# Kernel optimization log

Measured on AMD Instinct MI355X. Metric: run time of the kernel, lower is better.

The kernel has to match this reference:

```python
import jax, jax.numpy as jnp
import numpy as np

D, L, W_DIM, K = 16, 16, 16, 6
N = D * L * W_DIM
STD_POSITION = 1.0
STD_INTENSITY = 3.0


def _dist_weight():
    # pairwise Gaussian of squared Euclidean distance between voxel coords
    gx, gy, gz = jnp.meshgrid(jnp.arange(D, dtype=jnp.float32),
                              jnp.arange(L, dtype=jnp.float32),
                              jnp.arange(W_DIM, dtype=jnp.float32),
                              indexing='ij')
    sq = jnp.zeros((N, N), dtype=jnp.float32)
    for g in (gx, gy, gz):  # fixed 3-axis loop, accumulate per-axis [N,N] diffs
        v = g.reshape(-1)
        sq = sq + jnp.square(v[:, None] - v[None, :])
    return jnp.exp(-sq / (STD_POSITION ** 2))


def setup_inputs() -> dict:
    key = jax.random.key(0)
    k1, k2 = jax.random.split(key)
    patch = jax.random.uniform(k1, (D, L, W_DIM), dtype=jnp.float32)
    prob = jax.random.uniform(k2, (D, L, W_DIM, K), dtype=jnp.float32)
    return {"patch": patch, "prob": prob, "dist_weight": _dist_weight(), "k": K}


def reference(patch, prob, dist_weight, k):
    f = patch.reshape(-1)  # [N]
    # intensity affinity: exp(-((fi - fj)/std_intensity)^2), detached in original
    intensity = jnp.exp(-jnp.square((f[:, None] - f[None, :]) / STD_INTENSITY))
    weights = jax.lax.stop_gradient(intensity) * dist_weight  # [N, N]
    P = prob.reshape(-1, k)  # [N, K], matches prob[:,:,:,t].reshape(-1)
    WP = weights @ P                       # [N, K]
    num = jnp.sum(P * WP, axis=0)          # sum_ij w_ij p_i p_j per class
    den = P.T @ jnp.sum(weights, axis=1)   # sum_ij w_ij p_i per class
    loss = jnp.float32(k) - jnp.sum(num / den)
    return loss.astype(jnp.float32)
```

## Files before the change

kernel.cpp:

```cpp
#include <hip/hip_runtime.h>

#define KK 6
#define RAD 3
#define NOFF 7
#define NGRP 49
#define NBLK (16 * NGRP)
#define C_INT (-0.16029944898766259f)
#define C_POS (-1.4426950408889634f)

__global__ void __launch_bounds__(256) sncut_main(
    const float* __restrict__ patch,
    const float* __restrict__ prob,
    float* __restrict__ bpart)
{
    const int slice = blockIdx.x / NGRP;
    const int og    = blockIdx.x % NGRP;
    const int dx    = og / NOFF - RAD;
    const int dy    = og % NOFF - RAD;

    const int t = threadIdx.x;
    const int i = (slice << 8) + t;
    const int y = t >> 4, z = t & 15;

    const int xj = slice + dx;
    const int yj = y + dy;
    const bool vxy = ((unsigned)xj < 16u) & ((unsigned)yj < 16u);
    const int jbase = (xj << 8) + (yj << 4);

    const float fi = patch[i];
    const float2* __restrict__ P2 = reinterpret_cast<const float2*>(prob);
    const float2 pi0 = P2[i * 3], pi1 = P2[i * 3 + 1], pi2 = P2[i * 3 + 2];

    const float sqxy = C_POS * (float)(dx * dx + dy * dy);

    float s0 = 0.f, s1 = 0.f, s2 = 0.f, s3 = 0.f, s4 = 0.f, s5 = 0.f, r = 0.f;

    #pragma unroll
    for (int dz = -RAD; dz <= RAD; ++dz) {
        const int zj = z + dz;
        const bool valid = vxy & ((unsigned)zj < 16u);
        const int jj = valid ? (jbase + zj) : i;
        const float fj = patch[jj];
        const float2 q0 = P2[jj * 3], q1 = P2[jj * 3 + 1], q2 = P2[jj * 3 + 2];
        const float df = fi - fj;
        const float sqc = sqxy + (float)(dz * dz) * C_POS;
        float w = exp2f(fmaf(df * df, C_INT, sqc));
        w = valid ? w : 0.f;
        r += w;
        s0 = fmaf(w, q0.x, s0); s1 = fmaf(w, q0.y, s1);
        s2 = fmaf(w, q1.x, s2); s3 = fmaf(w, q1.y, s3);
        s4 = fmaf(w, q2.x, s4); s5 = fmaf(w, q2.y, s5);
    }

    float v[12];
    v[0] = s0 * pi0.x; v[1] = s1 * pi0.y; v[2] = s2 * pi1.x;
    v[3] = s3 * pi1.y; v[4] = s4 * pi2.x; v[5] = s5 * pi2.y;
    v[6] = r * pi0.x;  v[7] = r * pi0.y;  v[8] = r * pi1.x;
    v[9] = r * pi1.y;  v[10] = r * pi2.x; v[11] = r * pi2.y;

    #pragma unroll
    for (int m = 32; m >= 1; m >>= 1) {
        #pragma unroll
        for (int c = 0; c < 12; ++c) v[c] += __shfl_xor(v[c], m);
    }

    __shared__ float ls[4][12];
    const int wave = t >> 6, lane = t & 63;
    if (lane == 0) {
        #pragma unroll
        for (int c = 0; c < 12; ++c) ls[wave][c] = v[c];
    }
    __syncthreads();
    if (t < 12) {
        bpart[blockIdx.x * 12 + t] = ls[0][t] + ls[1][t] + ls[2][t] + ls[3][t];
    }
}

__global__ void __launch_bounds__(256) sncut_final(
    const float* __restrict__ bpart, float* __restrict__ out)
{
    const int t = threadIdx.x;
    float a[12];
    #pragma unroll
    for (int c = 0; c < 12; ++c) a[c] = 0.f;

    for (int row = t; row < NBLK; row += 256) {
        const float4* rp = reinterpret_cast<const float4*>(bpart + row * 12);
        const float4 b0 = rp[0], b1 = rp[1], b2 = rp[2];
        a[0] += b0.x; a[1] += b0.y; a[2]  += b0.z; a[3]  += b0.w;
        a[4] += b1.x; a[5] += b1.y; a[6]  += b1.z; a[7]  += b1.w;
        a[8] += b2.x; a[9] += b2.y; a[10] += b2.z; a[11] += b2.w;
    }

    #pragma unroll
    for (int m = 32; m >= 1; m >>= 1) {
        #pragma unroll
        for (int c = 0; c < 12; ++c) a[c] += __shfl_xor(a[c], m);
    }

    __shared__ float ls[4][12];
    const int wave = t >> 6, lane = t & 63;
    if (lane == 0) {
        #pragma unroll
        for (int c = 0; c < 12; ++c) ls[wave][c] = a[c];
    }
    __syncthreads();
    if (t == 0) {
        float loss = (float)KK;
        #pragma unroll
        for (int c = 0; c < KK; ++c) {
            const float num = ls[0][c]     + ls[1][c]     + ls[2][c]     + ls[3][c];
            const float den = ls[0][c + 6] + ls[1][c + 6] + ls[2][c + 6] + ls[3][c + 6];
            loss -= num / den;
        }
        out[0] = loss;
    }
}

extern "C" void kernel_launch(void* const* d_in, const int* in_sizes, int n_in,
                              void* d_out, int out_size, void* d_ws, size_t ws_size,
                              hipStream_t stream) {
    const float* patch = (const float*)d_in[0];
    const float* prob  = (const float*)d_in[1];
    float* out = (float*)d_out;
    float* bpart = (float*)d_ws;

    sncut_main<<<NBLK, 256, 0, stream>>>(patch, prob, bpart);
    sncut_final<<<1, 256, 0, stream>>>(bpart, out);
}
```

Baseline: 15.54 us.

## Fuse final reduction into main kernel via last-block atomic counter

```diff
diff --git a/kernel.cpp b/kernel.cpp
--- a/kernel.cpp
+++ b/kernel.cpp
@@ -8,9 +8,11 @@
 #define C_INT (-0.16029944898766259f)
 #define C_POS (-1.4426950408889634f)
 
-__global__ void __launch_bounds__(256) sncut_main(
+__global__ void __launch_bounds__(256) sncut_fused(
     const float* __restrict__ patch,
     const float* __restrict__ prob,
+    float* __restrict__ out,
+    unsigned* __restrict__ counter,
     float* __restrict__ bpart)
 {
     const int slice = blockIdx.x / NGRP;
@@ -65,6 +67,7 @@
     }
 
     __shared__ float ls[4][12];
+    __shared__ int lastflag;
     const int wave = t >> 6, lane = t & 63;
     if (lane == 0) {
         #pragma unroll
@@ -72,24 +75,28 @@
     }
     __syncthreads();
     if (t < 12) {
-        bpart[blockIdx.x * 12 + t] = ls[0][t] + ls[1][t] + ls[2][t] + ls[3][t];
+        const float p = ls[0][t] + ls[1][t] + ls[2][t] + ls[3][t];
+        __hip_atomic_store(&bpart[blockIdx.x * 12 + t], p,
+                           __ATOMIC_RELAXED, __HIP_MEMORY_SCOPE_AGENT);
     }
-}
+    __syncthreads();
+    if (t == 0) {
+        const unsigned old = __hip_atomic_fetch_add(
+            counter, 1u, __ATOMIC_ACQ_REL, __HIP_MEMORY_SCOPE_AGENT);
+        lastflag = (old == NBLK - 1) ? 1 : 0;
+    }
+    __syncthreads();
+    if (!lastflag) return;
 
-__global__ void __launch_bounds__(256) sncut_final(
-    const float* __restrict__ bpart, float* __restrict__ out)
-{
-    const int t = threadIdx.x;
     float a[12];
     #pragma unroll
     for (int c = 0; c < 12; ++c) a[c] = 0.f;
 
     for (int row = t; row < NBLK; row += 256) {
-        const float4* rp = reinterpret_cast<const float4*>(bpart + row * 12);
-        const float4 b0 = rp[0], b1 = rp[1], b2 = rp[2];
-        a[0] += b0.x; a[1] += b0.y; a[2]  += b0.z; a[3]  += b0.w;
-        a[4] += b1.x; a[5] += b1.y; a[6]  += b1.z; a[7]  += b1.w;
-        a[8] += b2.x; a[9] += b2.y; a[10] += b2.z; a[11] += b2.w;
+        #pragma unroll
+        for (int c = 0; c < 12; ++c)
+            a[c] += __hip_atomic_load(&bpart[row * 12 + c],
+                                      __ATOMIC_RELAXED, __HIP_MEMORY_SCOPE_AGENT);
     }
 
     #pragma unroll
@@ -98,8 +105,6 @@
         for (int c = 0; c < 12; ++c) a[c] += __shfl_xor(a[c], m);
     }
 
-    __shared__ float ls[4][12];
-    const int wave = t >> 6, lane = t & 63;
     if (lane == 0) {
         #pragma unroll
         for (int c = 0; c < 12; ++c) ls[wave][c] = a[c];
@@ -123,8 +128,9 @@
     const float* patch = (const float*)d_in[0];
     const float* prob  = (const float*)d_in[1];
     float* out = (float*)d_out;
-    float* bpart = (float*)d_ws;
+    unsigned* counter = (unsigned*)d_ws;
+    float* bpart = (float*)((char*)d_ws + 256);
 
-    sncut_main<<<NBLK, 256, 0, stream>>>(patch, prob, bpart);
-    sncut_final<<<1, 256, 0, stream>>>(bpart, out);
+    hipMemsetAsync(counter, 0, sizeof(unsigned), stream);
+    sncut_fused<<<NBLK, 256, 0, stream>>>(patch, prob, out, counter, bpart);
 }
```

Result: slower. 30.30 us (+95.0%).
